# Optimization experiments

Hardware: AMD Instinct MI355X
Metric: run time of the kernel (lower is better)

## Reference

```python
import jax, jax.numpy as jnp
import numpy as np

B, T, D_IN, H, D_ENC, P, D_ATT = 64, 20, 512, 512, 2048, 196, 512


def setup_inputs() -> dict:
    key = jax.random.key(0)
    ks = jax.random.split(key, 12)
    s = 0.05  # weight scale to keep gates out of saturation
    return {
        "x": jax.random.normal(ks[0], (B, T, D_IN), jnp.float32),
        "cnn_features": jax.random.normal(ks[1], (B, P, D_ENC), jnp.float32),
        "Wi": jax.random.normal(ks[2], (D_IN + H + D_ENC, H), jnp.float32) * s,
        "bi": jnp.zeros((H,), jnp.float32),
        "Wf": jax.random.normal(ks[3], (D_IN + H + D_ENC, H), jnp.float32) * s,
        "bf": jnp.zeros((H,), jnp.float32),
        "Wc": jax.random.normal(ks[4], (D_IN + H + D_ENC, H), jnp.float32) * s,
        "bc": jnp.zeros((H,), jnp.float32),
        "Wo": jax.random.normal(ks[5], (D_IN + H + D_ENC, H), jnp.float32) * s,
        "bo": jnp.zeros((H,), jnp.float32),
        "Wa_feat": jax.random.normal(ks[6], (D_ENC, D_ATT), jnp.float32) * s,
        "Wa_h": jax.random.normal(ks[7], (H, D_ATT), jnp.float32) * s,
        "ba": jnp.zeros((D_ATT,), jnp.float32),
        "v": jax.random.normal(ks[8], (D_ATT,), jnp.float32) * s,
    }


def reference(x, cnn_features, Wi, bi, Wf, bf, Wc, bc, Wo, bo, Wa_feat, Wa_h, ba, v):
    batch, seq_len, _ = x.shape
    hid = Wi.shape[1]
    # feature projection is h-independent: hoist out of the time loop
    feat_proj = jnp.einsum('bpe,ea->bpa', cnn_features, Wa_feat) + ba  # [B,P,A]

    def step(carry, x_t):
        h, c = carry
        # additive (Bahdanau) attention over pixels
        e = jnp.einsum('bpa,a->bp', jnp.tanh(feat_proj + (h @ Wa_h)[:, None, :]), v)
        alpha = jax.nn.softmax(e, axis=-1)                      # [B,P]
        ctx = jnp.einsum('bp,bpe->be', alpha, cnn_features)     # [B,E]
        comb = jnp.concatenate([x_t, h, ctx], axis=1)           # [B,D_IN+H+E]
        i_t = jax.nn.sigmoid(comb @ Wi + bi)
        f_t = jax.nn.sigmoid(comb @ Wf + bf)
        o_t = jax.nn.sigmoid(comb @ Wo + bo)
        c_tilde = jnp.tanh(comb @ Wc + bc)
        c_new = f_t * c + i_t * c_tilde
        h_new = o_t * jnp.tanh(c_new)
        return (h_new, c_new), h_new

    h0 = jnp.zeros((batch, hid), x.dtype)
    c0 = jnp.zeros((batch, hid), x.dtype)
    (h_T, c_T), ys = jax.lax.scan(step, (h0, c0), jnp.swapaxes(x, 0, 1))
    outputs = jnp.swapaxes(ys, 0, 1)  # [B,T,H]
    return outputs, h_T, c_T
```

## Files before the change

kernel.cpp:

```cpp
#include <hip/hip_runtime.h>

typedef unsigned short u16;
typedef unsigned int u32;
typedef __attribute__((ext_vector_type(8))) short bf16x8;
typedef __attribute__((ext_vector_type(4))) float f32x4;

#define NB 64
#define NT 20
#define NH 512
#define NP 196
#define NE 2048
#define NA 512

__device__ __forceinline__ u16 f2bf(float f) {
  u32 b = __float_as_uint(f);
  return (u16)((b + 0x7FFFu + ((b >> 16) & 1u)) >> 16);
}
__device__ __forceinline__ float bf2f(u16 u) { return __uint_as_float(((u32)u) << 16); }
__device__ __forceinline__ float tanh_fast(float x) {
  float xc = fminf(fmaxf(x, -15.f), 15.f);
  float e2 = __builtin_amdgcn_exp2f(xc * 2.885390082f);
  return (e2 - 1.f) * __builtin_amdgcn_rcpf(e2 + 1.f);
}
__device__ __forceinline__ float sigmoid_fast(float x) {
  return __builtin_amdgcn_rcpf(1.f + __builtin_amdgcn_exp2f(x * -1.44269504f));
}

__device__ __forceinline__ void gload_lds16(const u16* g, u16* l) {
  __builtin_amdgcn_global_load_lds((const __attribute__((address_space(1))) void*)g,
                                   (__attribute__((address_space(3))) void*)l, 16, 0, 0);
}

template <int N>
__device__ __forceinline__ void vwait() {
  if constexpr (N >= 0)
    asm volatile("s_waitcnt vmcnt(%0)" ::"i"(N) : "memory");
  else
    asm volatile("" ::: "memory");
}

__global__ __launch_bounds__(256) void conv_bf16(const float4* __restrict__ src,
                                                 u16* __restrict__ dst, int n4) {
  int i = blockIdx.x * 256 + threadIdx.x;
  int stride = gridDim.x * 256;
  for (; i < n4; i += stride) {
    float4 v = src[i];
    u32 lo = (u32)f2bf(v.x) | ((u32)f2bf(v.y) << 16);
    u32 hi = (u32)f2bf(v.z) | ((u32)f2bf(v.w) << 16);
    *(uint2*)(dst + (size_t)i * 4) = make_uint2(lo, hi);
  }
}

__global__ __launch_bounds__(128) void conv_x(const float* __restrict__ x,
                                              u16* __restrict__ xbT) {
  int b = blockIdx.x, t = blockIdx.y, tid = threadIdx.x;
  float4 v = *(const float4*)(x + ((size_t)b * NT + t) * 512 + tid * 4);
  u32 lo = (u32)f2bf(v.x) | ((u32)f2bf(v.y) << 16);
  u32 hi = (u32)f2bf(v.z) | ((u32)f2bf(v.w) << 16);
  *(uint2*)(xbT + ((size_t)t * NB + b) * 512 + tid * 4) = make_uint2(lo, hi);
}

__global__ __launch_bounds__(256) void transpose_all(
    const float* __restrict__ Wi, const float* __restrict__ Wf, const float* __restrict__ Wc,
    const float* __restrict__ Wo, const float* __restrict__ Waf, const float* __restrict__ Wah,
    u16* __restrict__ wxt, u16* __restrict__ wbig, u16* __restrict__ wcombT) {
  const int blk = blockIdx.x;
  const float* src;
  u16* dst;
  int row_off, K, bx, by;
  if (blk < 1024) {
    int z = blk >> 8, r = blk & 255;
    bx = r & 15;
    by = r >> 4;
    src = z == 0 ? Wi : z == 1 ? Wf : z == 2 ? Wc : Wo;
    dst = wxt + (size_t)z * 512 * 512;
    row_off = 0;
    K = 512;
  } else if (blk < 2048) {
    int r = blk - 1024;
    bx = r & 63;
    by = r >> 6;
    src = Waf;
    dst = wbig;
    row_off = 0;
    K = 2048;
  } else if (blk < 6144) {
    int r = blk - 2048;
    int z = r >> 10, r2 = r & 1023;
    bx = r2 & 63;
    by = r2 >> 6;
    src = z == 0 ? Wi : z == 1 ? Wf : z == 2 ? Wc : Wo;
    dst = wbig + (size_t)512 * 2048 + (size_t)z * 512 * 2048;
    row_off = 1024;
    K = 2048;
  } else if (blk < 7168) {
    int r = blk - 6144;
    int z = r >> 8, r2 = r & 255;
    bx = r2 & 15;
    by = r2 >> 4;
    src = z == 0 ? Wi : z == 1 ? Wf : z == 2 ? Wc : Wo;
    dst = wcombT + (size_t)z * 512 * 512;
    row_off = 512;
    K = 512;
  } else {
    int r = blk - 7168;
    bx = r & 15;
    by = r >> 4;
    src = Wah;
    dst = wcombT + (size_t)2048 * 512;
    row_off = 0;
    K = 512;
  }
  __shared__ float tile[32][33];
  const int k0 = bx * 32, n0 = by * 32;
  const int tx = threadIdx.x & 31, ty = threadIdx.x >> 5;
#pragma unroll
  for (int i = 0; i < 4; ++i)
    tile[ty + i * 8][tx] = src[(size_t)(row_off + k0 + ty + i * 8) * 512 + n0 + tx];
  __syncthreads();
#pragma unroll
  for (int i = 0; i < 4; ++i) {
    int n = n0 + ty + i * 8, k = k0 + tx;
    dst[(size_t)n * K + k] = f2bf(tile[tx][ty + i * 8]);
  }
}

__global__ __launch_bounds__(256) void gemm_bf16(const u16* __restrict__ A,
                                                 const u16* __restrict__ BT,
                                                 float* __restrict__ C, int M, int N, int K) {
  __shared__ u16 lA[128 * 64];
  __shared__ u16 lB[128 * 64];
  const int tid = threadIdx.x;
  const int lane = tid & 63;
  const int wid = tid >> 6;
  const int m0 = blockIdx.x * 128, n0 = blockIdx.y * 128;
  const int wm = (wid >> 1) * 64, wn = (wid & 1) * 64;
  f32x4 acc[4][4] = {};

  const int cbase = wid * 256;
  int srcr[4], srcc[4];
#pragma unroll
  for (int it = 0; it < 4; ++it) {
    int c = cbase + it * 64 + lane;
    srcr[it] = c >> 3;
    srcc[it] = ((c & 7) ^ ((c >> 3) & 7)) * 8;
  }

  for (int k0 = 0; k0 < K; k0 += 64) {
    __syncthreads();
#pragma unroll
    for (int it = 0; it < 4; ++it) {
      gload_lds16(A + (size_t)(m0 + srcr[it]) * K + k0 + srcc[it],
                  lA + (size_t)(cbase + it * 64) * 8);
      gload_lds16(BT + (size_t)(n0 + srcr[it]) * K + k0 + srcc[it],
                  lB + (size_t)(cbase + it * 64) * 8);
    }
    __syncthreads();
#pragma unroll
    for (int kk = 0; kk < 2; ++kk) {
      int kchunk = kk * 4 + (lane >> 4);
      bf16x8 af[4], bg[4];
#pragma unroll
      for (int i = 0; i < 4; ++i) {
        int row = wm + i * 16 + (lane & 15);
        af[i] = *(const bf16x8*)(lA + row * 64 + ((kchunk ^ (row & 7)) * 8));
        int rowb = wn + i * 16 + (lane & 15);
        bg[i] = *(const bf16x8*)(lB + rowb * 64 + ((kchunk ^ (rowb & 7)) * 8));
      }
#pragma unroll
      for (int i = 0; i < 4; ++i)
#pragma unroll
        for (int j = 0; j < 4; ++j)
          acc[i][j] = __builtin_amdgcn_mfma_f32_16x16x32_bf16(af[i], bg[j], acc[i][j], 0, 0, 0);
    }
  }
#pragma unroll
  for (int i = 0; i < 4; ++i) {
    int m = m0 + wm + i * 16 + ((lane >> 4) * 4);
#pragma unroll
    for (int j = 0; j < 4; ++j) {
      int n = n0 + wn + j * 16 + (lane & 15);
#pragma unroll
      for (int r = 0; r < 4; ++r) C[(size_t)(m + r) * N + n] = acc[i][j][r];
    }
  }
}

#define STG(SS, CUR, K1)                                                                    \
  do {                                                                                      \
    _Pragma("unroll") for (int q_ = 0; q_ < 2; ++q_) {                                      \
      const u16* g_ = ((SS) < 2)                                                            \
                          ? (A + (size_t)(m0 + sR[SS][q_]) * K + (K1) + sC[SS][q_])         \
                          : (BT + (size_t)(n0 + sR[SS][q_]) * K + (K1) + sC[SS][q_]);       \
      gload_lds16(g_, lds + ((CUR) ^ 1) * 32768 + sL[SS][q_]);                              \
    }                                                                                       \
  } while (0)

#define PH(MF0, READB, CUR, DOSTAGE, SB, K1, WN)                                            \
  do {                                                                                      \
    const u16* pA_ = lds + (CUR) * 32768;                                                   \
    const u16* pB_ = pA_ + 16384;                                                           \
    bf16x8 af_[2][2];                                                                       \
    _Pragma("unroll") for (int kh_ = 0; kh_ < 2; ++kh_) {                                   \
      const int kc_ = kh_ * 4 + (lane >> 4);                                                \
      _Pragma("unroll") for (int ii_ = 0; ii_ < 2; ++ii_) {                                 \
        const int rA_ = wmH * 128 + ((MF0) + ii_) * 16 + l15;                               \
        af_[kh_][ii_] = *(const bf16x8*)(pA_ + rA_ * 64 + ((kc_ ^ (rA_ & 7)) * 8));         \
      }                                                                                     \
      if (READB) {                                                                          \
        _Pragma("unroll") for (int j_ = 0; j_ < 4; ++j_) {                                  \
          const int rB_ = wnq * 64 + j_ * 16 + l15;                                         \
          bg[kh_][j_] = *(const bf16x8*)(pB_ + rB_ * 64 + ((kc_ ^ (rB_ & 7)) * 8));         \
        }                                                                                   \
      }                                                                                     \
    }                                                                                       \
    if (DOSTAGE) {                                                                          \
      STG(SB, CUR, K1);                                                                     \
      STG((SB) + 1, CUR, K1);                                                               \
    }                                                                                       \
    vwait<WN>();                                                                            \
    __builtin_amdgcn_s_barrier();                                                           \
    __builtin_amdgcn_s_setprio(1);                                                          \
    _Pragma("unroll") for (int kh_ = 0; kh_ < 2; ++kh_)                                     \
      _Pragma("unroll") for (int ii_ = 0; ii_ < 2; ++ii_)                                   \
        _Pragma("unroll") for (int j_ = 0; j_ < 4; ++j_)                                    \
          acc[(MF0) + ii_][j_] = __builtin_amdgcn_mfma_f32_16x16x32_bf16(                   \
              af_[kh_][ii_], bg[kh_][j_], acc[(MF0) + ii_][j_], 0, 0, 0);                   \
    __builtin_amdgcn_s_setprio(0);                                                          \
    __builtin_amdgcn_s_barrier();                                                           \
  } while (0)

__global__ __launch_bounds__(512, 2) void gemm256(const u16* __restrict__ A,
                                                  const u16* __restrict__ BT,
                                                  const float* __restrict__ bias,
                                                  u16* __restrict__ fpb, u16* __restrict__ cnW,
                                                  int K, int grid_n) {
  __shared__ u16 lds[65536];
  const int tid = threadIdx.x;
  const int lane = tid & 63;
  const int wid = tid >> 6;
  const int l15 = lane & 15;
  const int nblk = gridDim.x;
  const int q = nblk >> 3, rr = nblk & 7;
  const int xcd = blockIdx.x & 7, jj = blockIdx.x >> 3;
  const int swz = (xcd < rr ? xcd * (q + 1) : rr * (q + 1) + (xcd - rr) * q) + jj;
  const int mt = swz / grid_n, nt = swz - mt * grid_n;
  const int m0 = mt * 256, n0 = nt * 256;
  const int wmH = wid >> 2;
  const int wnq = wid & 3;
  f32x4 acc[8][4] = {};
  bf16x8 bg[2][4];

  int sR[4][2], sC[4][2], sL[4][2];
#pragma unroll
  for (int s = 0; s < 4; ++s)
#pragma unroll
    for (int qq = 0; qq < 2; ++qq) {
      int reg = (s < 2) ? s : s - 2;
      int ra = reg * 1024 + qq * 512 + wid * 64;
      int idx = ra + lane;
      sR[s][qq] = idx >> 3;
      sC[s][qq] = ((idx & 7) ^ ((idx >> 3) & 7)) * 8;
      sL[s][qq] = ((s < 2) ? 0 : 16384) + ra * 8;
    }

  STG(0, 1, 0);
  STG(1, 1, 0);
  STG(2, 1, 0);
  STG(3, 1, 0);
  vwait<0>();
  __builtin_amdgcn_s_barrier();

  const int KT = K >> 6;
  for (int kt = 0; kt < KT - 1; ++kt) {
    const int cur = kt & 1;
    const int k1 = (kt + 1) << 6;
    PH(0, 1, cur, 1, 0, k1, -1);
    PH(2, 0, cur, 1, 2, k1, -1);
    PH(4, 0, cur, 0, 0, 0, -1);
    PH(6, 0, cur, 0, 0, 0, 0);
  }
  {
    const int cur = (KT - 1) & 1;
    PH(0, 1, cur, 0, 0, 0, -1);
    PH(2, 0, cur, 0, 0, 0, -1);
    PH(4, 0, cur, 0, 0, 0, -1);
    PH(6, 0, cur, 0, 0, 0, -1);
  }

#pragma unroll
  for (int i = 0; i < 8; ++i) {
    int m = m0 + wmH * 128 + i * 16 + ((lane >> 4) * 4);
#pragma unroll
    for (int j = 0; j < 4; ++j) {
      int n = n0 + wnq * 64 + j * 16 + l15;
      float bv = (n < 512) ? bias[n] : 0.f;
#pragma unroll
      for (int r = 0; r < 4; ++r) {
        float val = acc[i][j][r] + bv;
        u32 me = (u32)(m + r);
        if (n < 512) {
          fpb[(size_t)me * 512 + n] = f2bf(val);
        } else {
          u32 bdx = me / 196u;
          u32 p = me - bdx * 196u;
          u32 g = (u32)(n - 512) >> 9;
          u32 n9 = (u32)(n - 512) & 511u;
          cnW[(((size_t)bdx * 4 + g) * 196 + p) * 512 + n9] = f2bf(val);
        }
      }
    }
  }
}

__global__ __launch_bounds__(256) void hproj(const u16* __restrict__ hprev,
                                             const u16* __restrict__ wcT,
                                             float* __restrict__ hp) {
  const int ntile = blockIdx.x;
  const int tid = threadIdx.x, lane = tid & 63, kh = tid >> 6;
  const int l15 = lane & 15;
  const u16* Bp = wcT + (size_t)(ntile * 16 + l15) * 512 + kh * 128 + ((lane >> 4) * 8);
  const u16* Ap = hprev + (size_t)l15 * 512 + kh * 128 + ((lane >> 4) * 8);
  f32x4 acc[4] = {};
#pragma unroll
  for (int ks = 0; ks < 4; ++ks) {
    bf16x8 bb = *(const bf16x8*)(Bp + ks * 32);
#pragma unroll
    for (int mf = 0; mf < 4; ++mf) {
      bf16x8 a = *(const bf16x8*)(Ap + (size_t)mf * 16 * 512 + ks * 32);
      acc[mf] = __builtin_amdgcn_mfma_f32_16x16x32_bf16(a, bb, acc[mf], 0, 0, 0);
    }
  }
  __shared__ float pre[4][64][16];
  const int rrow = (lane >> 4) * 4;
#pragma unroll
  for (int mf = 0; mf < 4; ++mf)
#pragma unroll
    for (int r = 0; r < 4; ++r) pre[kh][mf * 16 + rrow + r][l15] = acc[mf][r];
  __syncthreads();
  const int m = tid >> 2, n = (tid & 3) * 4;
  float4 s;
  float* sp = (float*)&s;
#pragma unroll
  for (int j = 0; j < 4; ++j)
    sp[j] = pre[0][m][n + j] + pre[1][m][n + j] + pre[2][m][n + j] + pre[3][m][n + j];
  *(float4*)(hp + (size_t)m * 2560 + ntile * 16 + n) = s;
}

__global__ __launch_bounds__(1024) void attn_gates(
    const u16* __restrict__ fpb, const float* __restrict__ hp, const float* __restrict__ v,
    const u16* __restrict__ cw, const float* __restrict__ xw, const float* __restrict__ bi,
    const float* __restrict__ bfg, const float* __restrict__ bc, const float* __restrict__ bo,
    float* __restrict__ cbuf, float* __restrict__ out, u16* __restrict__ hnext, int t) {
  const int b = blockIdx.x & 63;
  const int quarter = blockIdx.x >> 6;
  const int tid = threadIdx.x;
  const int lane = tid & 63, wid = tid >> 6;
  __shared__ float smem_a[1024];
  __shared__ float sm[16];
  __shared__ float alp[200];
  __shared__ float red[8192];

  float* hwa = smem_a;
  float* vv = smem_a + 512;
  if (tid < 512) {
    hwa[tid] = (t > 0) ? hp[(size_t)b * 2560 + 2048 + tid] : 0.f;
    vv[tid] = v[tid];
  }
  if (tid >= 196 && tid < 256) red[tid] = -3e38f;
  __syncthreads();

  float hw[8], vr[8];
#pragma unroll
  for (int j = 0; j < 8; ++j) {
    hw[j] = hwa[lane * 8 + j];
    vr[j] = vv[lane * 8 + j];
  }
  for (int p = wid; p < NP; p += 16) {
    const u16* fp = fpb + ((size_t)b * NP + p) * 512 + lane * 8;
    uint4 raw = *(const uint4*)fp;
    u32 w[4] = {raw.x, raw.y, raw.z, raw.w};
    float part = 0.f;
#pragma unroll
    for (int j = 0; j < 8; ++j) {
      u16 u = (u16)(w[j >> 1] >> ((j & 1) * 16));
      part += tanh_fast(bf2f(u) + hw[j]) * vr[j];
    }
#pragma unroll
    for (int off = 32; off > 0; off >>= 1) part += __shfl_xor(part, off);
    if (lane == 0) red[p] = part;
  }
  __syncthreads();

  float ev = 0.f, w = 0.f;
  if (tid < 256) {
    ev = red[tid];
    float m_ = ev;
#pragma unroll
    for (int off = 32; off > 0; off >>= 1) m_ = fmaxf(m_, __shfl_xor(m_, off));
    if (lane == 0) sm[wid] = m_;
  }
  __syncthreads();
  if (tid < 256) {
    float mx = fmaxf(fmaxf(sm[0], sm[1]), fmaxf(sm[2], sm[3]));
    w = (tid < NP) ? __builtin_amdgcn_exp2f((ev - mx) * 1.44269504f) : 0.f;
    float s_ = w;
#pragma unroll
    for (int off = 32; off > 0; off >>= 1) s_ += __shfl_xor(s_, off);
    if (lane == 0) sm[8 + wid] = s_;
  }
  __syncthreads();
  if (tid < NP) {
    float tot = (sm[8] + sm[9]) + (sm[10] + sm[11]);
    alp[tid] = w * __builtin_amdgcn_rcpf(tot);
  }
  __syncthreads();

  {
    const int g = tid >> 8, pg = (tid >> 4) & 15, colc = tid & 15;
    const u16* base = cw + ((size_t)(b * 4 + g) * 196) * 512 + quarter * 128 + colc * 8;
    float acc[8] = {};
    for (int i = 0; i < 13; ++i) {
      int p = pg + i * 16;
      if (p < NP) {
        float al = alp[p];
        uint4 raw = *(const uint4*)(base + (size_t)p * 512);
        u32 wds[4] = {raw.x, raw.y, raw.z, raw.w};
#pragma unroll
        for (int j = 0; j < 8; ++j) acc[j] += al * bf2f((u16)(wds[j >> 1] >> ((j & 1) * 16)));
      }
    }
#pragma unroll
    for (int j = 0; j < 8; ++j) red[((g * 16 + pg) * 16 + colc) * 8 + j] = acc[j];
  }
  __syncthreads();

  float* pre4 = smem_a;
  if (tid < 512) {
    const int gg = tid >> 7, nn = tid & 127;
    float s = 0.f;
#pragma unroll
    for (int pg2 = 0; pg2 < 16; ++pg2)
      s += red[((gg * 16 + pg2) * 16 + (nn >> 3)) * 8 + (nn & 7)];
    pre4[gg * 128 + nn] = s;
  }
  __syncthreads();

  if (tid < 128) {
    const int ng = quarter * 128 + tid;
    const size_t xwo = ((size_t)t * NB + b) * 2048;
    const size_t hpb = (size_t)b * 2560;
    float hwh0 = 0.f, hwh1 = 0.f, hwh2 = 0.f, hwh3 = 0.f;
    if (t > 0) {
      hwh0 = hp[hpb + ng];
      hwh1 = hp[hpb + 512 + ng];
      hwh2 = hp[hpb + 1024 + ng];
      hwh3 = hp[hpb + 1536 + ng];
    }
    float ip = pre4[0 * 128 + tid] + xw[xwo + ng] + hwh0 + bi[ng];
    float fp = pre4[1 * 128 + tid] + xw[xwo + 512 + ng] + hwh1 + bfg[ng];
    float cp = pre4[2 * 128 + tid] + xw[xwo + 1024 + ng] + hwh2 + bc[ng];
    float op = pre4[3 * 128 + tid] + xw[xwo + 1536 + ng] + hwh3 + bo[ng];
    float it = sigmoid_fast(ip), ft = sigmoid_fast(fp), ot = sigmoid_fast(op);
    float ctl = tanh_fast(cp);
    float cold = (t > 0) ? cbuf[(size_t)b * 512 + ng] : 0.f;
    float cn = ft * cold + it * ctl;
    float hn = ot * tanh_fast(cn);
    cbuf[(size_t)b * 512 + ng] = cn;
    hnext[(size_t)b * 512 + ng] = f2bf(hn);
    out[((size_t)b * NT + t) * 512 + ng] = hn;
    if (t == NT - 1) {
      out[(size_t)NB * NT * 512 + (size_t)b * 512 + ng] = hn;
      out[(size_t)NB * NT * 512 + (size_t)NB * 512 + (size_t)b * 512 + ng] = cn;
    }
  }
}

extern "C" void kernel_launch(void* const* d_in, const int* in_sizes, int n_in, void* d_out,
                              int out_size, void* d_ws, size_t ws_size, hipStream_t stream) {
  const float* x = (const float*)d_in[0];
  const float* cnn = (const float*)d_in[1];
  const float* Wi = (const float*)d_in[2];
  const float* bi = (const float*)d_in[3];
  const float* Wf = (const float*)d_in[4];
  const float* bfv = (const float*)d_in[5];
  const float* Wc = (const float*)d_in[6];
  const float* bc = (const float*)d_in[7];
  const float* Wo = (const float*)d_in[8];
  const float* bo = (const float*)d_in[9];
  const float* Waf = (const float*)d_in[10];
  const float* Wah = (const float*)d_in[11];
  const float* ba = (const float*)d_in[12];
  const float* v = (const float*)d_in[13];
  float* out = (float*)d_out;

  char* base = (char*)d_ws;
  size_t off = 0;
  auto alloc = [&](size_t bytes) {
    char* r = base + off;
    off += (bytes + 255) & ~(size_t)255;
    return r;
  };
  u16* cnnb = (u16*)alloc((size_t)NB * NP * NE * 2);
  u16* fpb = (u16*)alloc((size_t)NB * NP * NA * 2);
  u16* cnW = (u16*)alloc((size_t)NB * 4 * NP * 512 * 2);
  u16* wbig = (u16*)alloc((size_t)2560 * 2048 * 2);
  u16* wcombT = (u16*)alloc((size_t)2560 * 512 * 2);
  u16* wxt = (u16*)alloc((size_t)4 * 512 * 512 * 2);
  u16* xbT = (u16*)alloc((size_t)NT * NB * 512 * 2);
  float* xw = (float*)alloc((size_t)NT * NB * 2048 * 4);
  u16* hbuf = (u16*)alloc((size_t)2 * NB * 512 * 2);
  float* cbuf = (float*)alloc((size_t)NB * 512 * 4);
  float* hp = (float*)alloc((size_t)NB * 2560 * 4);

  (void)ws_size;
  (void)in_sizes;
  (void)n_in;
  (void)out_size;

  conv_bf16<<<2048, 256, 0, stream>>>((const float4*)cnn, cnnb, (NB * NP * NE) / 4);
  conv_x<<<dim3(NB, NT), 128, 0, stream>>>(x, xbT);
  transpose_all<<<7424, 256, 0, stream>>>(Wi, Wf, Wc, Wo, Waf, Wah, wxt, wbig, wcombT);

  gemm256<<<49 * 10, 512, 0, stream>>>(cnnb, wbig, ba, fpb, cnW, 2048, 10);

  {
    dim3 g(1280 / 128, 2048 / 128);
    gemm_bf16<<<g, 256, 0, stream>>>(xbT, wxt, xw, 1280, 2048, 512);
  }

  for (int t = 0; t < NT; ++t) {
    const u16* hprev = hbuf + (size_t)(t & 1) * NB * 512;
    u16* hnext = hbuf + (size_t)((t + 1) & 1) * NB * 512;
    if (t > 0) hproj<<<160, 256, 0, stream>>>(hprev, wcombT, hp);
    attn_gates<<<256, 1024, 0, stream>>>(fpb, hp, v, cnW, xw, bi, bfv, bc, bo, cbuf, out, hnext,
                                         t);
  }
}
```

Before: 669.1 us.

## Move attention scoring into hproj kernel and merge prep kernels

The three preprocessing kernels are merged into one launch. The per-step attention scores and softmax now run in the h-projection kernel, which gets 64 extra blocks, one per batch. Each of these blocks computes h·Wa_h itself with a scalar dot product, so it no longer waits on the MFMA projection. The attn_gates kernel then reads the precomputed alpha from a global buffer. This removes the scoring work that was repeated across the four quarter blocks of attn_gates, in exchange for a slow scalar 512x512 matvec per batch block and an extra global round trip for alpha.

```diff
diff --git a/kernel.cpp b/kernel.cpp
--- a/kernel.cpp
+++ b/kernel.cpp
@@ -39,53 +39,56 @@
     asm volatile("" ::: "memory");
 }
 
-__global__ __launch_bounds__(256) void conv_bf16(const float4* __restrict__ src,
-                                                 u16* __restrict__ dst, int n4) {
-  int i = blockIdx.x * 256 + threadIdx.x;
-  int stride = gridDim.x * 256;
-  for (; i < n4; i += stride) {
-    float4 v = src[i];
+__global__ __launch_bounds__(256) void prep_all(
+    const float4* __restrict__ cnn4, const float* __restrict__ x, const float* __restrict__ Wi,
+    const float* __restrict__ Wf, const float* __restrict__ Wc, const float* __restrict__ Wo,
+    const float* __restrict__ Waf, const float* __restrict__ Wah, u16* __restrict__ cnnb,
+    u16* __restrict__ xbT, u16* __restrict__ wxt, u16* __restrict__ wbig,
+    u16* __restrict__ wcombT) {
+  const int blk = blockIdx.x, tid = threadIdx.x;
+  __shared__ float tile[32][33];
+  if (blk < 2048) {
+    const int n4 = (NB * NP * NE) / 4;
+    for (int i = blk * 256 + tid; i < n4; i += 2048 * 256) {
+      float4 v = cnn4[i];
+      u32 lo = (u32)f2bf(v.x) | ((u32)f2bf(v.y) << 16);
+      u32 hi = (u32)f2bf(v.z) | ((u32)f2bf(v.w) << 16);
+      *(uint2*)(cnnb + (size_t)i * 4) = make_uint2(lo, hi);
+    }
+    return;
+  }
+  if (blk < 2688) {
+    const int j = (blk - 2048) * 256 + tid;
+    float4 v = ((const float4*)x)[j];
+    const int bt = j >> 7, c = j & 127;
+    const int b = bt / 20, t = bt - b * 20;
     u32 lo = (u32)f2bf(v.x) | ((u32)f2bf(v.y) << 16);
     u32 hi = (u32)f2bf(v.z) | ((u32)f2bf(v.w) << 16);
-    *(uint2*)(dst + (size_t)i * 4) = make_uint2(lo, hi);
-  }
-}
-
-__global__ __launch_bounds__(128) void conv_x(const float* __restrict__ x,
-                                              u16* __restrict__ xbT) {
-  int b = blockIdx.x, t = blockIdx.y, tid = threadIdx.x;
-  float4 v = *(const float4*)(x + ((size_t)b * NT + t) * 512 + tid * 4);
-  u32 lo = (u32)f2bf(v.x) | ((u32)f2bf(v.y) << 16);
-  u32 hi = (u32)f2bf(v.z) | ((u32)f2bf(v.w) << 16);
-  *(uint2*)(xbT + ((size_t)t * NB + b) * 512 + tid * 4) = make_uint2(lo, hi);
-}
-
-__global__ __launch_bounds__(256) void transpose_all(
-    const float* __restrict__ Wi, const float* __restrict__ Wf, const float* __restrict__ Wc,
-    const float* __restrict__ Wo, const float* __restrict__ Waf, const float* __restrict__ Wah,
-    u16* __restrict__ wxt, u16* __restrict__ wbig, u16* __restrict__ wcombT) {
-  const int blk = blockIdx.x;
+    *(uint2*)(xbT + ((size_t)t * NB + b) * 512 + c * 4) = make_uint2(lo, hi);
+    return;
+  }
+  const int tb = blk - 2688;
   const float* src;
   u16* dst;
   int row_off, K, bx, by;
-  if (blk < 1024) {
-    int z = blk >> 8, r = blk & 255;
+  if (tb < 1024) {
+    int z = tb >> 8, r = tb & 255;
     bx = r & 15;
     by = r >> 4;
     src = z == 0 ? Wi : z == 1 ? Wf : z == 2 ? Wc : Wo;
     dst = wxt + (size_t)z * 512 * 512;
     row_off = 0;
     K = 512;
-  } else if (blk < 2048) {
-    int r = blk - 1024;
+  } else if (tb < 2048) {
+    int r = tb - 1024;
     bx = r & 63;
     by = r >> 6;
     src = Waf;
     dst = wbig;
     row_off = 0;
     K = 2048;
-  } else if (blk < 6144) {
-    int r = blk - 2048;
+  } else if (tb < 6144) {
+    int r = tb - 2048;
     int z = r >> 10, r2 = r & 1023;
     bx = r2 & 63;
     by = r2 >> 6;
@@ -93,8 +96,8 @@
     dst = wbig + (size_t)512 * 2048 + (size_t)z * 512 * 2048;
     row_off = 1024;
     K = 2048;
-  } else if (blk < 7168) {
-    int r = blk - 6144;
+  } else if (tb < 7168) {
+    int r = tb - 6144;
     int z = r >> 8, r2 = r & 255;
     bx = r2 & 15;
     by = r2 >> 4;
@@ -103,7 +106,7 @@
     row_off = 512;
     K = 512;
   } else {
-    int r = blk - 7168;
+    int r = tb - 7168;
     bx = r & 15;
     by = r >> 4;
     src = Wah;
@@ -111,9 +114,8 @@
     row_off = 0;
     K = 512;
   }
-  __shared__ float tile[32][33];
   const int k0 = bx * 32, n0 = by * 32;
-  const int tx = threadIdx.x & 31, ty = threadIdx.x >> 5;
+  const int tx = tid & 31, ty = tid >> 5;
 #pragma unroll
   for (int i = 0; i < 4; ++i)
     tile[ty + i * 8][tx] = src[(size_t)(row_off + k0 + ty + i * 8) * 512 + n0 + tx];
@@ -313,61 +315,76 @@
   }
 }
 
-__global__ __launch_bounds__(256) void hproj(const u16* __restrict__ hprev,
-                                             const u16* __restrict__ wcT,
-                                             float* __restrict__ hp) {
-  const int ntile = blockIdx.x;
-  const int tid = threadIdx.x, lane = tid & 63, kh = tid >> 6;
-  const int l15 = lane & 15;
-  const u16* Bp = wcT + (size_t)(ntile * 16 + l15) * 512 + kh * 128 + ((lane >> 4) * 8);
-  const u16* Ap = hprev + (size_t)l15 * 512 + kh * 128 + ((lane >> 4) * 8);
-  f32x4 acc[4] = {};
-#pragma unroll
-  for (int ks = 0; ks < 4; ++ks) {
-    bf16x8 bb = *(const bf16x8*)(Bp + ks * 32);
-#pragma unroll
-    for (int mf = 0; mf < 4; ++mf) {
-      bf16x8 a = *(const bf16x8*)(Ap + (size_t)mf * 16 * 512 + ks * 32);
-      acc[mf] = __builtin_amdgcn_mfma_f32_16x16x32_bf16(a, bb, acc[mf], 0, 0, 0);
-    }
-  }
-  __shared__ float pre[4][64][16];
-  const int rrow = (lane >> 4) * 4;
-#pragma unroll
-  for (int mf = 0; mf < 4; ++mf)
-#pragma unroll
-    for (int r = 0; r < 4; ++r) pre[kh][mf * 16 + rrow + r][l15] = acc[mf][r];
-  __syncthreads();
-  const int m = tid >> 2, n = (tid & 3) * 4;
-  float4 s;
-  float* sp = (float*)&s;
-#pragma unroll
-  for (int j = 0; j < 4; ++j)
-    sp[j] = pre[0][m][n + j] + pre[1][m][n + j] + pre[2][m][n + j] + pre[3][m][n + j];
-  *(float4*)(hp + (size_t)m * 2560 + ntile * 16 + n) = s;
-}
-
-__global__ __launch_bounds__(1024) void attn_gates(
-    const u16* __restrict__ fpb, const float* __restrict__ hp, const float* __restrict__ v,
-    const u16* __restrict__ cw, const float* __restrict__ xw, const float* __restrict__ bi,
-    const float* __restrict__ bfg, const float* __restrict__ bc, const float* __restrict__ bo,
-    float* __restrict__ cbuf, float* __restrict__ out, u16* __restrict__ hnext, int t) {
-  const int b = blockIdx.x & 63;
-  const int quarter = blockIdx.x >> 6;
-  const int tid = threadIdx.x;
-  const int lane = tid & 63, wid = tid >> 6;
-  __shared__ float smem_a[1024];
+__global__ __launch_bounds__(256) void hproj_attn(
+    const u16* __restrict__ hprev, const u16* __restrict__ wcT, float* __restrict__ hp,
+    const u16* __restrict__ fpb, const float* __restrict__ v, float* __restrict__ albuf,
+    int t) {
+  const int tid = threadIdx.x, lane = tid & 63, wid = tid >> 6;
+  if (blockIdx.x < 128) {
+    if (t == 0) return;
+    const int ntile = blockIdx.x;
+    const int kh = wid;
+    const int l15 = lane & 15;
+    const u16* Bp = wcT + (size_t)(ntile * 16 + l15) * 512 + kh * 128 + ((lane >> 4) * 8);
+    const u16* Ap = hprev + (size_t)l15 * 512 + kh * 128 + ((lane >> 4) * 8);
+    f32x4 acc[4] = {};
+#pragma unroll
+    for (int ks = 0; ks < 4; ++ks) {
+      bf16x8 bb = *(const bf16x8*)(Bp + ks * 32);
+#pragma unroll
+      for (int mf = 0; mf < 4; ++mf) {
+        bf16x8 a = *(const bf16x8*)(Ap + (size_t)mf * 16 * 512 + ks * 32);
+        acc[mf] = __builtin_amdgcn_mfma_f32_16x16x32_bf16(a, bb, acc[mf], 0, 0, 0);
+      }
+    }
+    __shared__ float pre[4][64][16];
+    const int rrow = (lane >> 4) * 4;
+#pragma unroll
+    for (int mf = 0; mf < 4; ++mf)
+#pragma unroll
+      for (int r = 0; r < 4; ++r) pre[kh][mf * 16 + rrow + r][l15] = acc[mf][r];
+    __syncthreads();
+    const int m = tid >> 2, n = (tid & 3) * 4;
+    float4 s;
+    float* sp = (float*)&s;
+#pragma unroll
+    for (int j = 0; j < 4; ++j)
+      sp[j] = pre[0][m][n + j] + pre[1][m][n + j] + pre[2][m][n + j] + pre[3][m][n + j];
+    *(float4*)(hp + (size_t)m * 2560 + ntile * 16 + n) = s;
+    return;
+  }
+
+  const int b = blockIdx.x - 128;
+  __shared__ float hl[512];
+  __shared__ float hwa[512];
+  __shared__ float vv[512];
+  __shared__ float elds[256];
   __shared__ float sm[16];
-  __shared__ float alp[200];
-  __shared__ float red[8192];
-
-  float* hwa = smem_a;
-  float* vv = smem_a + 512;
-  if (tid < 512) {
-    hwa[tid] = (t > 0) ? hp[(size_t)b * 2560 + 2048 + tid] : 0.f;
-    vv[tid] = v[tid];
-  }
-  if (tid >= 196 && tid < 256) red[tid] = -3e38f;
+  hl[tid] = bf2f(hprev[(size_t)b * 512 + tid]);
+  hl[tid + 256] = bf2f(hprev[(size_t)b * 512 + tid + 256]);
+  vv[tid] = v[tid];
+  vv[tid + 256] = v[tid + 256];
+  if (tid >= 196) elds[tid] = -3e38f;
+  __syncthreads();
+  {
+    float a0 = 0.f, a1 = 0.f;
+    if (t > 0) {
+      const u16* w0 = wcT + (size_t)(2048 + tid) * 512;
+      const u16* w1 = w0 + (size_t)256 * 512;
+      for (int k = 0; k < 512; k += 8) {
+        bf16x8 wv0 = *(const bf16x8*)(w0 + k);
+        bf16x8 wv1 = *(const bf16x8*)(w1 + k);
+#pragma unroll
+        for (int j = 0; j < 8; ++j) {
+          float hk = hl[k + j];
+          a0 += hk * bf2f((u16)wv0[j]);
+          a1 += hk * bf2f((u16)wv1[j]);
+        }
+      }
+    }
+    hwa[tid] = a0;
+    hwa[tid + 256] = a1;
+  }
   __syncthreads();
 
   float hw[8], vr[8];
@@ -376,7 +393,7 @@
     hw[j] = hwa[lane * 8 + j];
     vr[j] = vv[lane * 8 + j];
   }
-  for (int p = wid; p < NP; p += 16) {
+  for (int p = wid; p < NP; p += 4) {
     const u16* fp = fpb + ((size_t)b * NP + p) * 512 + lane * 8;
     uint4 raw = *(const uint4*)fp;
     u32 w[4] = {raw.x, raw.y, raw.z, raw.w};
@@ -388,32 +405,42 @@
     }
 #pragma unroll
     for (int off = 32; off > 0; off >>= 1) part += __shfl_xor(part, off);
-    if (lane == 0) red[p] = part;
-  }
-  __syncthreads();
-
-  float ev = 0.f, w = 0.f;
-  if (tid < 256) {
-    ev = red[tid];
-    float m_ = ev;
-#pragma unroll
-    for (int off = 32; off > 0; off >>= 1) m_ = fmaxf(m_, __shfl_xor(m_, off));
-    if (lane == 0) sm[wid] = m_;
-  }
-  __syncthreads();
-  if (tid < 256) {
-    float mx = fmaxf(fmaxf(sm[0], sm[1]), fmaxf(sm[2], sm[3]));
-    w = (tid < NP) ? __builtin_amdgcn_exp2f((ev - mx) * 1.44269504f) : 0.f;
-    float s_ = w;
-#pragma unroll
-    for (int off = 32; off > 0; off >>= 1) s_ += __shfl_xor(s_, off);
-    if (lane == 0) sm[8 + wid] = s_;
-  }
+    if (lane == 0) elds[p] = part;
+  }
+  __syncthreads();
+
+  float ev = elds[tid];
+  float m_ = ev;
+#pragma unroll
+  for (int off = 32; off > 0; off >>= 1) m_ = fmaxf(m_, __shfl_xor(m_, off));
+  if (lane == 0) sm[wid] = m_;
+  __syncthreads();
+  float mx = fmaxf(fmaxf(sm[0], sm[1]), fmaxf(sm[2], sm[3]));
+  float w = (tid < NP) ? __builtin_amdgcn_exp2f((ev - mx) * 1.44269504f) : 0.f;
+  float s_ = w;
+#pragma unroll
+  for (int off = 32; off > 0; off >>= 1) s_ += __shfl_xor(s_, off);
+  if (lane == 0) sm[8 + wid] = s_;
   __syncthreads();
   if (tid < NP) {
     float tot = (sm[8] + sm[9]) + (sm[10] + sm[11]);
-    alp[tid] = w * __builtin_amdgcn_rcpf(tot);
-  }
+    albuf[(size_t)b * 256 + tid] = w * __builtin_amdgcn_rcpf(tot);
+  }
+}
+
+__global__ __launch_bounds__(1024) void attn_gates(
+    const float* __restrict__ albuf, const float* __restrict__ hp, const u16* __restrict__ cw,
+    const float* __restrict__ xw, const float* __restrict__ bi, const float* __restrict__ bfg,
+    const float* __restrict__ bc, const float* __restrict__ bo, float* __restrict__ cbuf,
+    float* __restrict__ out, u16* __restrict__ hnext, int t) {
+  const int b = blockIdx.x & 63;
+  const int quarter = blockIdx.x >> 6;
+  const int tid = threadIdx.x;
+  __shared__ float pre4[512];
+  __shared__ float alp[200];
+  __shared__ float red[8192];
+
+  if (tid < NP) alp[tid] = albuf[(size_t)b * 256 + tid];
   __syncthreads();
 
   {
@@ -435,7 +462,6 @@
   }
   __syncthreads();
 
-  float* pre4 = smem_a;
   if (tid < 512) {
     const int gg = tid >> 7, nn = tid & 127;
     float s = 0.f;
@@ -512,15 +538,15 @@
   u16* hbuf = (u16*)alloc((size_t)2 * NB * 512 * 2);
   float* cbuf = (float*)alloc((size_t)NB * 512 * 4);
   float* hp = (float*)alloc((size_t)NB * 2560 * 4);
+  float* albuf = (float*)alloc((size_t)NB * 256 * 4);
 
   (void)ws_size;
   (void)in_sizes;
   (void)n_in;
   (void)out_size;
 
-  conv_bf16<<<2048, 256, 0, stream>>>((const float4*)cnn, cnnb, (NB * NP * NE) / 4);
-  conv_x<<<dim3(NB, NT), 128, 0, stream>>>(x, xbT);
-  transpose_all<<<7424, 256, 0, stream>>>(Wi, Wf, Wc, Wo, Waf, Wah, wxt, wbig, wcombT);
+  prep_all<<<10112, 256, 0, stream>>>((const float4*)cnn, x, Wi, Wf, Wc, Wo, Waf, Wah, cnnb, xbT,
+                                      wxt, wbig, wcombT);
 
   gemm256<<<49 * 10, 512, 0, stream>>>(cnnb, wbig, ba, fpb, cnW, 2048, 10);
 
@@ -532,8 +558,8 @@
   for (int t = 0; t < NT; ++t) {
     const u16* hprev = hbuf + (size_t)(t & 1) * NB * 512;
     u16* hnext = hbuf + (size_t)((t + 1) & 1) * NB * 512;
-    if (t > 0) hproj<<<160, 256, 0, stream>>>(hprev, wcombT, hp);
-    attn_gates<<<256, 1024, 0, stream>>>(fpb, hp, v, cnW, xw, bi, bfv, bc, bo, cbuf, out, hnext,
+    hproj_attn<<<192, 256, 0, stream>>>(hprev, wcombT, hp, fpb, v, albuf, t);
+    attn_gates<<<256, 1024, 0, stream>>>(albuf, hp, cnW, xw, bi, bfv, bc, bo, cbuf, out, hnext,
                                          t);
   }
 }
```

New measurement: 1.341 ms. +100.4%, slower.
